# Optimization experiments

Measured on AMD Instinct MI355X. Metric: run time of the kernel, lower is better.

## Reference

```python
import jax, jax.numpy as jnp
import numpy as np

A, G, P, C = 250000, 64, 4096, 2
LOW, HIGH = 0.3, 0.7
BETA = 1.0 / 9.0
IMG = 800.0


def _make_boxes(key, n):
    k1, k2 = jax.random.split(key)
    xy = jax.random.uniform(k1, (n, 2), minval=0.0, maxval=IMG - 130.0)
    wh = jax.random.uniform(k2, (n, 2), minval=8.0, maxval=128.0)
    return jnp.concatenate([xy, xy + wh], axis=1)


def setup_inputs():
    ks = jax.random.split(jax.random.key(0), 11)
    return {
        "anchors": _make_boxes(ks[0], A),
        "gt_boxes": _make_boxes(ks[1], G),
        "gt_score_labels": jax.random.uniform(ks[2], (G,)),
        "gt_confidence_labels": jax.random.randint(ks[3], (G,), 0, 2),
        "objectness": jax.random.normal(ks[4], (A,)),
        "pred_bbox_deltas": jax.random.normal(ks[5], (A, 4)) * 0.1,
        "class_logits": jax.random.normal(ks[6], (P, C)),
        "box_regression": jax.random.normal(ks[7], (P, C * 4)) * 0.1,
        "roi_labels": jax.random.randint(ks[8], (P,), 0, C),
        "roi_regression_targets": jax.random.normal(ks[9], (P, 4)) * 0.1,
        "roi_scores": jax.random.uniform(ks[10], (P,)),
    }


def box_iou(a, b):
    # a: [G,4], b: [A,4] -> [G,A]
    area_a = (a[:, 2] - a[:, 0]) * (a[:, 3] - a[:, 1])
    area_b = (b[:, 2] - b[:, 0]) * (b[:, 3] - b[:, 1])
    lt = jnp.maximum(a[:, None, :2], b[None, :, :2])
    rb = jnp.minimum(a[:, None, 2:], b[None, :, 2:])
    wh = jnp.clip(rb - lt, 0.0)
    inter = wh[..., 0] * wh[..., 1]
    return inter / (area_a[:, None] + area_b[None, :] - inter)


def encode_boxes(gt, anchors):
    # torchvision BoxCoder.encode with unit weights
    aw = anchors[:, 2] - anchors[:, 0]
    ah = anchors[:, 3] - anchors[:, 1]
    acx = anchors[:, 0] + 0.5 * aw
    acy = anchors[:, 1] + 0.5 * ah
    gw = gt[:, 2] - gt[:, 0]
    gh = gt[:, 3] - gt[:, 1]
    gcx = gt[:, 0] + 0.5 * gw
    gcy = gt[:, 1] + 0.5 * gh
    return jnp.stack([(gcx - acx) / aw, (gcy - acy) / ah,
                      jnp.log(gw / aw), jnp.log(gh / ah)], axis=1)


def smooth_l1(d):
    ad = jnp.abs(d)
    return jnp.where(ad < BETA, 0.5 * d * d / BETA, ad - 0.5 * BETA)


def reference(anchors, gt_boxes, gt_score_labels, gt_confidence_labels, objectness,
              pred_bbox_deltas, class_logits, box_regression, roi_labels,
              roi_regression_targets, roi_scores):
    # ---- assign_targets_to_anchors (Matcher with low-quality matches) ----
    iou = box_iou(gt_boxes, anchors)            # [G, A]
    matched_vals = iou.max(axis=0)              # [A]
    all_matches = iou.argmax(axis=0)            # [A]
    matched_idxs = jnp.where(matched_vals < LOW, -1,
                   jnp.where(matched_vals < HIGH, -2, all_matches))
    best_per_gt = iou.max(axis=1, keepdims=True)            # [G,1]
    force = (iou == best_per_gt).any(axis=0)                # [A]
    matched_idxs = jnp.where(force, all_matches, matched_idxs)
    clamped = jnp.clip(matched_idxs, 0)
    matched_gt = gt_boxes[clamped]                          # [A,4]
    labels = (matched_idxs >= 0).astype(jnp.float32)
    labels = jnp.minimum(labels, gt_score_labels[clamped])
    labels = jnp.where(matched_idxs == -1, 0.0, labels)     # BELOW_LOW_THRESHOLD
    labels = jnp.where(matched_idxs == -2, -1.0, labels)    # BETWEEN_THRESHOLDS
    labels = jnp.where((gt_confidence_labels[clamped] == 0) & (matched_idxs >= 0), -1.0, labels)
    reg_targets = encode_boxes(matched_gt, anchors)         # [A,4]

    # ---- my_rpn_compute_loss (deterministic full pos/neg selection) ----
    pos = labels >= 1.0
    neg = labels == 0.0
    n_samp = pos.astype(jnp.float32).sum() + neg.astype(jnp.float32).sum()
    sl = smooth_l1(pred_bbox_deltas - reg_targets).sum(axis=-1)
    rpn_box_loss = (sl * pos).sum() / n_samp
    sel = pos | neg
    y = jnp.where(sel, jnp.clip(labels, 0.0, 1.0), 0.0)
    x = objectness
    bce = jnp.maximum(x, 0.0) - x * y + jnp.log1p(jnp.exp(-jnp.abs(x)))
    objectness_loss = (bce * sel).sum() / n_samp

    # ---- my_roi_loss ----
    fixed_labels = jnp.stack([1.0 - roi_scores, roi_scores], axis=1)  # [P,2]
    log_probs = jax.nn.log_softmax(class_logits, axis=1)
    classification_loss = jnp.mean(-(fixed_labels * log_probs).sum(axis=1))
    br = box_regression.reshape(P, C, 4)
    idx = jnp.broadcast_to(jnp.clip(roi_labels, 0)[:, None, None], (P, 1, 4))
    br_sel = jnp.take_along_axis(br, idx, axis=1)[:, 0]               # [P,4]
    pos_roi = (roi_labels > 0).astype(jnp.float32)
    roi_box_loss = (smooth_l1(br_sel - roi_regression_targets).sum(axis=-1) * pos_roi).sum() / P

    return jnp.stack([objectness_loss, rpn_box_loss, classification_loss, roi_box_loss])
```

## Files before the change

kernel.cpp:

```cpp
#include <hip/hip_runtime.h>
#include <hip/hip_bf16.h>
#include <math.h>

#define NA 250000
#define NG 64
#define NP 4096

#define SLICES 64
#define SLICE_SPAN 4096
#define GPB 4
#define GGRP (NG / GPB)
#define P1_BLOCKS (SLICES * GGRP)
#define ABLK ((NA + 255) / 256)
#define RBLK (NP / 256)

#define OFF_GTP  0
#define OFF_BEST 512
#define OFF_SUM  (512 + NG * SLICES)
#define OFF_ROI  (OFF_SUM + ABLK * 4)


static __device__ __forceinline__ float iou_one(
    float gx0, float gy0, float gx1, float gy1, float ga,
    float ax0, float ay0, float ax1, float ay1, float aa)
{
#pragma clang fp contract(off)
    float ltx = fmaxf(gx0, ax0);
    float lty = fmaxf(gy0, ay0);
    float rbx = fminf(gx1, ax1);
    float rby = fminf(gy1, ay1);
    float w = fmaxf(rbx - ltx, 0.0f);
    float h = fmaxf(rby - lty, 0.0f);
    float inter = w * h;
    float uni = ga + aa - inter;
    return inter * __builtin_amdgcn_rcpf(uni);
}

static __device__ __forceinline__ float smooth_l1_f(float d) {
    const float BETA = 1.0f / 9.0f;
    float ad = fabsf(d);
    return (ad < BETA) ? (0.5f * d * d / BETA) : (ad - 0.5f * BETA);
}


__global__ __launch_bounds__(256) void k_pass1(const float4* __restrict__ anchors,
                                               const float4* __restrict__ gt,
                                               const float* __restrict__ gscore,
                                               const int* __restrict__ gconf,
                                               float* __restrict__ ws) {
    int t = threadIdx.x;
    if (blockIdx.x == P1_BLOCKS) {
        if (t < NG) {
            float4 g = gt[t];
            float* r = ws + OFF_GTP + 8 * t;
            r[0] = g.x; r[1] = g.y; r[2] = g.z; r[3] = g.w;
            r[4] = (g.z - g.x) * (g.w - g.y);
            r[6] = gscore[t];
            r[7] = (float)gconf[t];
        }
        return;
    }
    __shared__ float swm[4][GPB];
    int slice = blockIdx.x & 63;
    int ggrp = blockIdx.x >> 6;
    int g0 = ggrp * GPB;

    float gx0[GPB], gy0[GPB], gx1[GPB], gy1[GPB], ga[GPB];
#pragma unroll
    for (int i = 0; i < GPB; i++) {
        float4 gb = gt[g0 + i];
        gx0[i] = gb.x; gy0[i] = gb.y; gx1[i] = gb.z; gy1[i] = gb.w;
        ga[i] = (gb.z - gb.x) * (gb.w - gb.y);
    }

    float m[GPB] = {0.f, 0.f, 0.f, 0.f};
    int base = slice * SLICE_SPAN + t;
#pragma unroll 4
    for (int k = 0; k < SLICE_SPAN / 256; k++) {
        int a = base + k * 256;
        float4 v = (a < NA) ? anchors[a] : make_float4(0.f, 0.f, 0.f, 0.f);
        float aa = (v.z - v.x) * (v.w - v.y);
#pragma unroll
        for (int i = 0; i < GPB; i++)
            m[i] = fmaxf(m[i], iou_one(gx0[i], gy0[i], gx1[i], gy1[i], ga[i],
                                       v.x, v.y, v.z, v.w, aa));
    }
    int lane = t & 63, w = t >> 6;
#pragma unroll
    for (int i = 0; i < GPB; i++) {
        float mm = m[i];
        for (int off = 32; off > 0; off >>= 1)
            mm = fmaxf(mm, __shfl_down(mm, off));
        if (lane == 0) swm[w][i] = mm;
    }
    __syncthreads();
    if (t < GPB) {
        float mm = fmaxf(fmaxf(swm[0][t], swm[1][t]), fmaxf(swm[2][t], swm[3][t]));
        ws[OFF_BEST + slice * NG + g0 + t] = mm;
    }
}

__global__ __launch_bounds__(64) void k_mid(float* __restrict__ ws) {
    int g = threadIdx.x;
    float mm = 0.f;
    for (int s = 0; s < SLICES; s++)
        mm = fmaxf(mm, ws[OFF_BEST + s * NG + g]);
    ws[OFF_GTP + 8 * g + 5] = mm;
}

__global__ __launch_bounds__(256) void k_main(const float4* __restrict__ anchors,
                                              const float* __restrict__ objness,
                                              const float4* __restrict__ pdel,
                                              const float* __restrict__ logits,
                                              const float* __restrict__ breg,
                                              const int* __restrict__ rlab,
                                              const float4* __restrict__ rtgt,
                                              const float* __restrict__ rsc,
                                              float* __restrict__ ws) {
    __shared__ float rbuf[4][4];
    int t = threadIdx.x;
    int lane = t & 63, w = t >> 6;
    const float* __restrict__ gtp = ws + OFF_GTP;

    if (blockIdx.x >= ABLK) {
        int p = (blockIdx.x - ABLK) * 256 + t;
        float clsl = 0.f, boxl = 0.f;
        {
            float l0 = logits[2 * p], l1 = logits[2 * p + 1];
            float mx = fmaxf(l0, l1);
            float lse = mx + logf(expf(l0 - mx) + expf(l1 - mx));
            float s = rsc[p];
            clsl = -((1.0f - s) * (l0 - lse) + s * (l1 - lse));

            int lbl = rlab[p];
            int cl = lbl < 0 ? 0 : lbl;
            float4 bb = *(const float4*)(breg + 8 * p + 4 * cl);
            float4 tg = rtgt[p];
            float sl = smooth_l1_f(bb.x - tg.x) + smooth_l1_f(bb.y - tg.y) +
                       smooth_l1_f(bb.z - tg.z) + smooth_l1_f(bb.w - tg.w);
            boxl = (lbl > 0) ? sl : 0.0f;
        }
        for (int off = 32; off > 0; off >>= 1) {
            clsl += __shfl_down(clsl, off);
            boxl += __shfl_down(boxl, off);
        }
        if (lane == 0) { rbuf[w][0] = clsl; rbuf[w][1] = boxl; }
        __syncthreads();
        if (t == 0) {
            float s0 = 0.f, s1 = 0.f;
            for (int i = 0; i < 4; i++) { s0 += rbuf[i][0]; s1 += rbuf[i][1]; }
            float* r = ws + OFF_ROI + 2 * (blockIdx.x - ABLK);
            r[0] = s0; r[1] = s1;
        }
        return;
    }

    int a = blockIdx.x * 256 + t;
    float posf = 0.f, negf = 0.f, slpos = 0.f, bces = 0.f;
    if (a < NA) {
        float4 av = anchors[a];
        float aarea = (av.z - av.x) * (av.w - av.y);
        float maxv = -1.0f;
        int arg = 0;
        bool force = false;
#pragma unroll 8
        for (int g = 0; g < NG; g++) {
            const float* G = gtp + 8 * g;
            float v = iou_one(G[0], G[1], G[2], G[3], G[4],
                              av.x, av.y, av.z, av.w, aarea);
            if (v > maxv) { maxv = v; arg = g; }
            force = force || (v == G[5]);
        }
        int matched = (maxv < 0.3f) ? -1 : ((maxv < 0.7f) ? -2 : arg);
        if (force) matched = arg;
        int cl = matched < 0 ? 0 : matched;

        const float* Gc = gtp + 8 * cl;
        float4 Ac = *(const float4*)Gc;
        float score = Gc[6], conf = Gc[7];
        float label = (matched >= 0) ? 1.0f : 0.0f;
        label = fminf(label, score);
        if (matched == -1) label = 0.0f;
        if (matched == -2) label = -1.0f;
        if (conf == 0.0f && matched >= 0) label = -1.0f;

        bool pos = (label >= 1.0f);
        bool neg = (label == 0.0f);
        bool sel = pos || neg;

        float aw = av.z - av.x, ah = av.w - av.y;
        float acx = av.x + 0.5f * aw, acy = av.y + 0.5f * ah;
        float gw = Ac.z - Ac.x, gh = Ac.w - Ac.y;
        float gcx = Ac.x + 0.5f * gw, gcy = Ac.y + 0.5f * gh;
        float t0 = (gcx - acx) / aw;
        float t1 = (gcy - acy) / ah;
        float t2 = logf(gw / aw);
        float t3 = logf(gh / ah);

        float4 pd = pdel[a];
        float sl = smooth_l1_f(pd.x - t0) + smooth_l1_f(pd.y - t1) +
                   smooth_l1_f(pd.z - t2) + smooth_l1_f(pd.w - t3);

        float x = objness[a];
        float y = sel ? fminf(fmaxf(label, 0.0f), 1.0f) : 0.0f;
        float bce = fmaxf(x, 0.0f) - x * y + log1pf(expf(-fabsf(x)));

        posf = pos ? 1.0f : 0.0f;
        negf = neg ? 1.0f : 0.0f;
        slpos = pos ? sl : 0.0f;
        bces = sel ? bce : 0.0f;
    }

    for (int off = 32; off > 0; off >>= 1) {
        posf  += __shfl_down(posf, off);
        negf  += __shfl_down(negf, off);
        slpos += __shfl_down(slpos, off);
        bces  += __shfl_down(bces, off);
    }
    if (lane == 0) { rbuf[w][0] = posf; rbuf[w][1] = negf; rbuf[w][2] = slpos; rbuf[w][3] = bces; }
    __syncthreads();
    if (t == 0) {
        float s0 = 0.f, s1 = 0.f, s2 = 0.f, s3 = 0.f;
        for (int i = 0; i < 4; i++) { s0 += rbuf[i][0]; s1 += rbuf[i][1]; s2 += rbuf[i][2]; s3 += rbuf[i][3]; }
        float* r = ws + OFF_SUM + 4 * blockIdx.x;
        r[0] = s0; r[1] = s1; r[2] = s2; r[3] = s3;
    }
}

__global__ __launch_bounds__(256) void k_fin(const float* __restrict__ ws,
                                             float* __restrict__ out) {
    __shared__ double sred[4][6];
    int t = threadIdx.x;
    int lane = t & 63, w = t >> 6;
    double a0 = 0, a1 = 0, a2 = 0, a3 = 0, c0 = 0, c1 = 0;
    for (int r = t; r < ABLK; r += 256) {
        const float4 v = *(const float4*)(ws + OFF_SUM + 4 * r);
        a0 += v.x; a1 += v.y; a2 += v.z; a3 += v.w;
    }
    if (t < RBLK) {
        c0 = ws[OFF_ROI + 2 * t];
        c1 = ws[OFF_ROI + 2 * t + 1];
    }
    for (int off = 32; off > 0; off >>= 1) {
        a0 += __shfl_down(a0, off);
        a1 += __shfl_down(a1, off);
        a2 += __shfl_down(a2, off);
        a3 += __shfl_down(a3, off);
        c0 += __shfl_down(c0, off);
        c1 += __shfl_down(c1, off);
    }
    if (lane == 0) {
        sred[w][0] = a0; sred[w][1] = a1; sred[w][2] = a2;
        sred[w][3] = a3; sred[w][4] = c0; sred[w][5] = c1;
    }
    __syncthreads();
    if (t == 0) {
        double s[6] = {0, 0, 0, 0, 0, 0};
        for (int i = 0; i < 4; i++)
            for (int j = 0; j < 6; j++) s[j] += sred[i][j];
        double n = s[0] + s[1];
        out[0] = (float)(s[3] / n);
        out[1] = (float)(s[2] / n);
        out[2] = (float)(s[4] / (double)NP);
        out[3] = (float)(s[5] / (double)NP);
    }
}

extern "C" void kernel_launch(void* const* d_in, const int* in_sizes, int n_in,
                              void* d_out, int out_size, void* d_ws, size_t ws_size,
                              hipStream_t stream) {
    const float4* anchors = (const float4*)d_in[0];
    const float4* gt      = (const float4*)d_in[1];
    const float*  gscore  = (const float*)d_in[2];
    const int*    gconf   = (const int*)d_in[3];
    const float*  objness = (const float*)d_in[4];
    const float4* pdel    = (const float4*)d_in[5];
    const float*  clog    = (const float*)d_in[6];
    const float*  breg    = (const float*)d_in[7];
    const int*    rlab    = (const int*)d_in[8];
    const float4* rtgt    = (const float4*)d_in[9];
    const float*  rsc     = (const float*)d_in[10];

    float* ws = (float*)d_ws;
    float* out = (float*)d_out;

    k_pass1<<<P1_BLOCKS + 1, 256, 0, stream>>>(anchors, gt, gscore, gconf, ws);
    k_mid<<<1, 64, 0, stream>>>(ws);
    k_main<<<ABLK + RBLK, 256, 0, stream>>>(anchors, objness, pdel, clog, breg,
                                            rlab, rtgt, rsc, ws);
    k_fin<<<1, 256, 0, stream>>>(ws, out);
}
```

Before: 119.9 us.

## Cut kernel launches from four to two via fused stages and atomic final reduction

Merges the ROI loss work into the first pass, folds the per-GT max reduction into each main block (reading a transposed best-IoU table from shared memory), and replaces the final reduction kernel with float atomics plus a last-block-done counter. The first pass now handles 8 GTs per block instead of 4. This is meant to remove two kernel launches and their inter-kernel gaps. In exchange, every main block redundantly re-reduces the 64x64 best table. Float atomic accumulation also makes the summation order nondeterministic.

```diff
diff --git a/kernel.cpp b/kernel.cpp
--- a/kernel.cpp
+++ b/kernel.cpp
@@ -6,18 +6,21 @@
 #define NG 64
 #define NP 4096
 
+#define GPB 8
+#define GGRP (NG / GPB)
 #define SLICES 64
 #define SLICE_SPAN 4096
-#define GPB 4
-#define GGRP (NG / GPB)
 #define P1_BLOCKS (SLICES * GGRP)
+#define RBLK (NP / 256)
+#define K1_BLOCKS (P1_BLOCKS + RBLK + 1)
+
 #define ABLK ((NA + 255) / 256)
-#define RBLK (NP / 256)
 
 #define OFF_GTP  0
-#define OFF_BEST 512
-#define OFF_SUM  (512 + NG * SLICES)
-#define OFF_ROI  (OFF_SUM + ABLK * 4)
+#define OFF_BEST (OFF_GTP + NG * 8)
+#define OFF_ROI  (OFF_BEST + NG * SLICES)
+#define OFF_ACC  (OFF_ROI + RBLK * 2)
+#define OFF_CNT  (OFF_ACC + 8)
 
 
 static __device__ __forceinline__ float iou_one(
@@ -43,26 +46,73 @@
 }
 
 
-__global__ __launch_bounds__(256) void k_pass1(const float4* __restrict__ anchors,
-                                               const float4* __restrict__ gt,
-                                               const float* __restrict__ gscore,
-                                               const int* __restrict__ gconf,
-                                               float* __restrict__ ws) {
+__global__ __launch_bounds__(256) void k1(const float4* __restrict__ anchors,
+                                          const float4* __restrict__ gt,
+                                          const float* __restrict__ gscore,
+                                          const int* __restrict__ gconf,
+                                          const float* __restrict__ logits,
+                                          const float* __restrict__ breg,
+                                          const int* __restrict__ rlab,
+                                          const float4* __restrict__ rtgt,
+                                          const float* __restrict__ rsc,
+                                          float* __restrict__ ws) {
     int t = threadIdx.x;
-    if (blockIdx.x == P1_BLOCKS) {
+    int b = blockIdx.x;
+
+    if (b == K1_BLOCKS - 1) {
         if (t < NG) {
             float4 g = gt[t];
             float* r = ws + OFF_GTP + 8 * t;
             r[0] = g.x; r[1] = g.y; r[2] = g.z; r[3] = g.w;
             r[4] = (g.z - g.x) * (g.w - g.y);
-            r[6] = gscore[t];
-            r[7] = (float)gconf[t];
+            r[5] = gscore[t];
+            r[6] = (float)gconf[t];
+            r[7] = 0.0f;
+        } else if (t < NG + 4) {
+            ws[OFF_ACC + (t - NG)] = 0.0f;
+        } else if (t == NG + 4) {
+            *(unsigned*)(ws + OFF_CNT) = 0u;
         }
         return;
     }
+
+    if (b >= P1_BLOCKS) {
+        __shared__ float rbuf[4][2];
+        int rb = b - P1_BLOCKS;
+        int p = rb * 256 + t;
+        float l0 = logits[2 * p], l1 = logits[2 * p + 1];
+        float mx = fmaxf(l0, l1);
+        float lse = mx + logf(expf(l0 - mx) + expf(l1 - mx));
+        float s = rsc[p];
+        float clsl = -((1.0f - s) * (l0 - lse) + s * (l1 - lse));
+
+        int lbl = rlab[p];
+        int cl = lbl < 0 ? 0 : lbl;
+        float4 bb = *(const float4*)(breg + 8 * p + 4 * cl);
+        float4 tg = rtgt[p];
+        float sl = smooth_l1_f(bb.x - tg.x) + smooth_l1_f(bb.y - tg.y) +
+                   smooth_l1_f(bb.z - tg.z) + smooth_l1_f(bb.w - tg.w);
+        float boxl = (lbl > 0) ? sl : 0.0f;
+
+        int lane = t & 63, w = t >> 6;
+        for (int off = 32; off > 0; off >>= 1) {
+            clsl += __shfl_down(clsl, off);
+            boxl += __shfl_down(boxl, off);
+        }
+        if (lane == 0) { rbuf[w][0] = clsl; rbuf[w][1] = boxl; }
+        __syncthreads();
+        if (t == 0) {
+            float s0 = 0.f, s1 = 0.f;
+            for (int i = 0; i < 4; i++) { s0 += rbuf[i][0]; s1 += rbuf[i][1]; }
+            ws[OFF_ROI + 2 * rb] = s0;
+            ws[OFF_ROI + 2 * rb + 1] = s1;
+        }
+        return;
+    }
+
     __shared__ float swm[4][GPB];
-    int slice = blockIdx.x & 63;
-    int ggrp = blockIdx.x >> 6;
+    int slice = b >> 3;
+    int ggrp = b & 7;
     int g0 = ggrp * GPB;
 
     float gx0[GPB], gy0[GPB], gx1[GPB], gy1[GPB], ga[GPB];
@@ -73,7 +123,10 @@
         ga[i] = (gb.z - gb.x) * (gb.w - gb.y);
     }
 
-    float m[GPB] = {0.f, 0.f, 0.f, 0.f};
+    float m[GPB];
+#pragma unroll
+    for (int i = 0; i < GPB; i++) m[i] = 0.0f;
+
     int base = slice * SLICE_SPAN + t;
 #pragma unroll 4
     for (int k = 0; k < SLICE_SPAN / 256; k++) {
@@ -96,64 +149,37 @@
     __syncthreads();
     if (t < GPB) {
         float mm = fmaxf(fmaxf(swm[0][t], swm[1][t]), fmaxf(swm[2][t], swm[3][t]));
-        ws[OFF_BEST + slice * NG + g0 + t] = mm;
-    }
-}
-
-__global__ __launch_bounds__(64) void k_mid(float* __restrict__ ws) {
-    int g = threadIdx.x;
-    float mm = 0.f;
-    for (int s = 0; s < SLICES; s++)
-        mm = fmaxf(mm, ws[OFF_BEST + s * NG + g]);
-    ws[OFF_GTP + 8 * g + 5] = mm;
-}
-
-__global__ __launch_bounds__(256) void k_main(const float4* __restrict__ anchors,
-                                              const float* __restrict__ objness,
-                                              const float4* __restrict__ pdel,
-                                              const float* __restrict__ logits,
-                                              const float* __restrict__ breg,
-                                              const int* __restrict__ rlab,
-                                              const float4* __restrict__ rtgt,
-                                              const float* __restrict__ rsc,
-                                              float* __restrict__ ws) {
+        ws[OFF_BEST + (g0 + t) * SLICES + slice] = mm;
+    }
+}
+
+
+__global__ __launch_bounds__(256) void k2(const float4* __restrict__ anchors,
+                                          const float* __restrict__ objness,
+                                          const float4* __restrict__ pdel,
+                                          float* __restrict__ ws,
+                                          float* __restrict__ out) {
+    __shared__ float sbest[NG];
+    __shared__ float red[NG][4];
     __shared__ float rbuf[4][4];
     int t = threadIdx.x;
     int lane = t & 63, w = t >> 6;
     const float* __restrict__ gtp = ws + OFF_GTP;
 
-    if (blockIdx.x >= ABLK) {
-        int p = (blockIdx.x - ABLK) * 256 + t;
-        float clsl = 0.f, boxl = 0.f;
-        {
-            float l0 = logits[2 * p], l1 = logits[2 * p + 1];
-            float mx = fmaxf(l0, l1);
-            float lse = mx + logf(expf(l0 - mx) + expf(l1 - mx));
-            float s = rsc[p];
-            clsl = -((1.0f - s) * (l0 - lse) + s * (l1 - lse));
-
-            int lbl = rlab[p];
-            int cl = lbl < 0 ? 0 : lbl;
-            float4 bb = *(const float4*)(breg + 8 * p + 4 * cl);
-            float4 tg = rtgt[p];
-            float sl = smooth_l1_f(bb.x - tg.x) + smooth_l1_f(bb.y - tg.y) +
-                       smooth_l1_f(bb.z - tg.z) + smooth_l1_f(bb.w - tg.w);
-            boxl = (lbl > 0) ? sl : 0.0f;
-        }
-        for (int off = 32; off > 0; off >>= 1) {
-            clsl += __shfl_down(clsl, off);
-            boxl += __shfl_down(boxl, off);
-        }
-        if (lane == 0) { rbuf[w][0] = clsl; rbuf[w][1] = boxl; }
-        __syncthreads();
-        if (t == 0) {
-            float s0 = 0.f, s1 = 0.f;
-            for (int i = 0; i < 4; i++) { s0 += rbuf[i][0]; s1 += rbuf[i][1]; }
-            float* r = ws + OFF_ROI + 2 * (blockIdx.x - ABLK);
-            r[0] = s0; r[1] = s1;
-        }
-        return;
-    }
+    {
+        int g = t >> 2, q = t & 3;
+        const float4* rp = (const float4*)(ws + OFF_BEST) + g * 16 + q * 4;
+        float4 v0 = rp[0], v1 = rp[1], v2 = rp[2], v3 = rp[3];
+        float mm = fmaxf(fmaxf(fmaxf(v0.x, v0.y), fmaxf(v0.z, v0.w)),
+                         fmaxf(fmaxf(v1.x, v1.y), fmaxf(v1.z, v1.w)));
+        mm = fmaxf(mm, fmaxf(fmaxf(fmaxf(v2.x, v2.y), fmaxf(v2.z, v2.w)),
+                             fmaxf(fmaxf(v3.x, v3.y), fmaxf(v3.z, v3.w))));
+        red[g][q] = mm;
+    }
+    __syncthreads();
+    if (t < NG)
+        sbest[t] = fmaxf(fmaxf(red[t][0], red[t][1]), fmaxf(red[t][2], red[t][3]));
+    __syncthreads();
 
     int a = blockIdx.x * 256 + t;
     float posf = 0.f, negf = 0.f, slpos = 0.f, bces = 0.f;
@@ -169,7 +195,7 @@
             float v = iou_one(G[0], G[1], G[2], G[3], G[4],
                               av.x, av.y, av.z, av.w, aarea);
             if (v > maxv) { maxv = v; arg = g; }
-            force = force || (v == G[5]);
+            force = force || (v == sbest[g]);
         }
         int matched = (maxv < 0.3f) ? -1 : ((maxv < 0.7f) ? -2 : arg);
         if (force) matched = arg;
@@ -177,7 +203,7 @@
 
         const float* Gc = gtp + 8 * cl;
         float4 Ac = *(const float4*)Gc;
-        float score = Gc[6], conf = Gc[7];
+        float score = Gc[4 + 1], conf = Gc[4 + 2];
         float label = (matched >= 0) ? 1.0f : 0.0f;
         label = fminf(label, score);
         if (matched == -1) label = 0.0f;
@@ -222,47 +248,30 @@
     if (t == 0) {
         float s0 = 0.f, s1 = 0.f, s2 = 0.f, s3 = 0.f;
         for (int i = 0; i < 4; i++) { s0 += rbuf[i][0]; s1 += rbuf[i][1]; s2 += rbuf[i][2]; s3 += rbuf[i][3]; }
-        float* r = ws + OFF_SUM + 4 * blockIdx.x;
-        r[0] = s0; r[1] = s1; r[2] = s2; r[3] = s3;
-    }
-}
-
-__global__ __launch_bounds__(256) void k_fin(const float* __restrict__ ws,
-                                             float* __restrict__ out) {
-    __shared__ double sred[4][6];
-    int t = threadIdx.x;
-    int lane = t & 63, w = t >> 6;
-    double a0 = 0, a1 = 0, a2 = 0, a3 = 0, c0 = 0, c1 = 0;
-    for (int r = t; r < ABLK; r += 256) {
-        const float4 v = *(const float4*)(ws + OFF_SUM + 4 * r);
-        a0 += v.x; a1 += v.y; a2 += v.z; a3 += v.w;
-    }
-    if (t < RBLK) {
-        c0 = ws[OFF_ROI + 2 * t];
-        c1 = ws[OFF_ROI + 2 * t + 1];
-    }
-    for (int off = 32; off > 0; off >>= 1) {
-        a0 += __shfl_down(a0, off);
-        a1 += __shfl_down(a1, off);
-        a2 += __shfl_down(a2, off);
-        a3 += __shfl_down(a3, off);
-        c0 += __shfl_down(c0, off);
-        c1 += __shfl_down(c1, off);
-    }
-    if (lane == 0) {
-        sred[w][0] = a0; sred[w][1] = a1; sred[w][2] = a2;
-        sred[w][3] = a3; sred[w][4] = c0; sred[w][5] = c1;
-    }
-    __syncthreads();
-    if (t == 0) {
-        double s[6] = {0, 0, 0, 0, 0, 0};
-        for (int i = 0; i < 4; i++)
-            for (int j = 0; j < 6; j++) s[j] += sred[i][j];
-        double n = s[0] + s[1];
-        out[0] = (float)(s[3] / n);
-        out[1] = (float)(s[2] / n);
-        out[2] = (float)(s[4] / (double)NP);
-        out[3] = (float)(s[5] / (double)NP);
+        float* acc = ws + OFF_ACC;
+        atomicAdd(&acc[0], s0);
+        atomicAdd(&acc[1], s1);
+        atomicAdd(&acc[2], s2);
+        atomicAdd(&acc[3], s3);
+        __threadfence();
+        unsigned old = atomicAdd((unsigned*)(ws + OFF_CNT), 1u);
+        if (old == ABLK - 1) {
+            __threadfence();
+            double c0 = 0.0, c1 = 0.0;
+            for (int i = 0; i < RBLK; i++) {
+                c0 += (double)ws[OFF_ROI + 2 * i];
+                c1 += (double)ws[OFF_ROI + 2 * i + 1];
+            }
+            double p  = (double)atomicAdd(&acc[0], 0.0f);
+            double n  = (double)atomicAdd(&acc[1], 0.0f);
+            double sl = (double)atomicAdd(&acc[2], 0.0f);
+            double bc = (double)atomicAdd(&acc[3], 0.0f);
+            double ns = p + n;
+            out[0] = (float)(bc / ns);
+            out[1] = (float)(sl / ns);
+            out[2] = (float)(c0 / (double)NP);
+            out[3] = (float)(c1 / (double)NP);
+        }
     }
 }
 
@@ -284,9 +293,7 @@
     float* ws = (float*)d_ws;
     float* out = (float*)d_out;
 
-    k_pass1<<<P1_BLOCKS + 1, 256, 0, stream>>>(anchors, gt, gscore, gconf, ws);
-    k_mid<<<1, 64, 0, stream>>>(ws);
-    k_main<<<ABLK + RBLK, 256, 0, stream>>>(anchors, objness, pdel, clog, breg,
-                                            rlab, rtgt, rsc, ws);
-    k_fin<<<1, 256, 0, stream>>>(ws, out);
-}
+    k1<<<K1_BLOCKS, 256, 0, stream>>>(anchors, gt, gscore, gconf, clog, breg,
+                                      rlab, rtgt, rsc, ws);
+    k2<<<ABLK, 256, 0, stream>>>(anchors, objness, pdel, ws, out);
+}
```

After: 168.9 us. 40.9% more time.
